# Kernel optimization log

Hardware: AMD Instinct MI355X
Metric: run time of the kernel (lower is better)

The kernel has to match this reference:

```python
import jax, jax.numpy as jnp
import numpy as np

B, T, K = 256, 1024, 128


def setup_inputs() -> dict:
    key = jax.random.key(0)
    k1, k2, k3, k4, k5 = jax.random.split(key, 5)
    EMISSIONS = jax.random.normal(k1, (B, T, K), dtype=jnp.float32)
    TAGS = jax.random.randint(k2, (B, T), 0, K, dtype=jnp.int64)
    MASK = jnp.ones((B, T), dtype=bool)
    START = jax.random.normal(k3, (K,), dtype=jnp.float32) * 0.01
    END = jax.random.normal(k4, (K,), dtype=jnp.float32) * 0.01
    TRANS = jax.random.normal(k5, (K, K), dtype=jnp.float32) * 0.01
    return {"EMISSIONS": EMISSIONS, "TAGS": TAGS, "MASK": MASK,
            "START": START, "END": END, "TRANS": TRANS}


def _forward_logz(emissions, mask, start, end, trans):
    # emissions (B,T,K), mask (B,T) bool -> logZ (B,)
    alpha0 = start[None, :] + emissions[:, 0, :]  # (B,K)

    def step(alpha, inp):
        emit, m = inp  # emit (B,K), m (B,) bool
        # PACK[b,i,j] = alpha[b,i] + trans[i,j]; logsumexp over prev tag i
        new = jax.nn.logsumexp(alpha[:, :, None] + trans[None, :, :], axis=1) + emit
        alpha = jnp.where(m[:, None], new, alpha)
        return alpha, None

    xs = (jnp.swapaxes(emissions[:, 1:, :], 0, 1),  # (T-1,B,K)
          jnp.swapaxes(mask[:, 1:], 0, 1))          # (T-1,B)
    alphaT, _ = jax.lax.scan(step, alpha0, xs)
    return jax.nn.logsumexp(alphaT + end[None, :], axis=1)


def _gold_score(emissions, tags, mask, start, end, trans):
    b = emissions.shape[0]
    ba = jnp.arange(b)
    maskf = mask.astype(emissions.dtype)
    sc0 = (start[tags[:, 0]] + emissions[ba, 0, tags[:, 0]]) * maskf[:, 0]
    pr = jnp.maximum(tags[:, :-1], 0)  # clamp(min=0)
    cr = jnp.maximum(tags[:, 1:], 0)
    m = (mask[:, 1:] & mask[:, :-1]).astype(emissions.dtype)  # (B,T-1)
    trans_sc = trans[pr, cr]  # (B,T-1)
    emit_sc = jnp.take_along_axis(emissions[:, 1:, :], cr[:, :, None], axis=2)[:, :, 0]
    sc = sc0 + jnp.sum((trans_sc + emit_sc) * m, axis=1)
    lenm1 = jnp.sum(mask.astype(jnp.int32), axis=1) - 1
    last = tags[ba, lenm1]
    return sc + end[last]


def reference(EMISSIONS, TAGS, MASK, START, END, TRANS):
    logz = _forward_logz(EMISSIONS, MASK, START, END, TRANS)
    gold = _gold_score(EMISSIONS, TAGS, MASK, START, END, TRANS)
    return jnp.mean(logz - gold)
```

## Files before the change

kernel.cpp:

```cpp
#include <hip/hip_runtime.h>
#include <math.h>

#define Bn 256
#define Tn 1024
#define Kn 128
#define NT 512
#define CH 16
#define CHF (CH * Kn)
#define USTR 36
#define UW (4 * USTR)

__device__ __forceinline__ float quad_reduce_add(float s) {
    int t = __builtin_amdgcn_mov_dpp(__float_as_int(s), 0xB1, 0xF, 0xF, true);
    s += __int_as_float(t);
    t = __builtin_amdgcn_mov_dpp(__float_as_int(s), 0x4E, 0xF, 0xF, true);
    s += __int_as_float(t);
    return s;
}

__global__ __launch_bounds__(NT, 2) void crf_fwd_kernel(
    const float* __restrict__ emis,
    const int*   __restrict__ tags,
    const float* __restrict__ startv,
    const float* __restrict__ endv,
    const float* __restrict__ trans,
    float* __restrict__ per_b)
{
    const int b    = blockIdx.x;
    const int tid  = threadIdx.x;
    const int wave = tid >> 6;
    const int lane = tid & 63;
    const int c    = wave * 16 + (lane >> 2);
    const int h    = lane & 3;

    __shared__ __align__(16) float U[2][UW];
    __shared__ __align__(16) float X[2][CHF];
    __shared__ float red[NT];

    const float* eb = emis + (size_t)b * Tn * Kn;
    const int*   tb = tags + b * Tn;

    const float* tp = trans + (size_t)(h * 32) * Kn + c;
    float4 E0, E1, E2, E3, E4, E5, E6, E7;
#define LDE(g, Eg)                                   \
    Eg.x = __expf(tp[(size_t)(4 * g + 0) * Kn]);     \
    Eg.y = __expf(tp[(size_t)(4 * g + 1) * Kn]);     \
    Eg.z = __expf(tp[(size_t)(4 * g + 2) * Kn]);     \
    Eg.w = __expf(tp[(size_t)(4 * g + 3) * Kn]);
    LDE(0, E0) LDE(1, E1) LDE(2, E2) LDE(3, E3)
    LDE(4, E4) LDE(5, E5) LDE(6, E6) LDE(7, E7)
#undef LDE

    float gl = 0.f;
    for (int t = 1 + tid; t < Tn; t += NT) {
        int pt = tb[t - 1];
        int ct = tb[t];
        gl += trans[pt * Kn + ct] + eb[(size_t)t * Kn + ct];
    }
    if (tid == 0) {
        int t0 = tb[0];
        gl += startv[t0] + eb[t0] + endv[tb[Tn - 1]];
    }
    red[tid] = gl;

    {
        const float4* e4 = (const float4*)(eb + Kn);
        ((float4*)X[0])[tid] = e4[tid];
    }
    if (tid < Kn) {
        U[1][(tid >> 5) * USTR + (tid & 31)] = __expf(startv[tid] + eb[tid]);
    }
    __syncthreads();

#pragma unroll
    for (int s = NT / 2; s > 0; s >>= 1) {
        if (tid < s) red[tid] += red[tid + s];
        __syncthreads();
    }
    const float gold = red[0];

    float  base = 0.f;
    float4 pf0  = make_float4(0, 0, 0, 0);
    const int urd = h * USTR;
    const int uwr = (c >> 5) * USTR + (c & 31);

    for (int r = 1; r < Tn; ++r) {
        const int tc   = r - 1;
        const int slot = tc & (CH - 1);
        const int cbuf = (tc >> 4) & 1;
        const int rb   = r & 1;
        const int wb   = rb ^ 1;

        if (slot == 0 && r + CH < Tn) {
            const float4* s4 = (const float4*)(eb + (size_t)(r + CH) * Kn);
            size_t base_el = (size_t)(r + CH) * Kn;
            pf0 = (base_el + (size_t)tid * 4 + 3 < (size_t)Tn * Kn)
                      ? s4[tid] : make_float4(0, 0, 0, 0);
        }
        if (slot == 8 && (r - 8) + CH < Tn) {
            ((float4*)X[cbuf ^ 1])[tid] = pf0;
        }

        const float4* Up = (const float4*)&U[rb][urd];
        float u0 = U[rb][0];
        float xr = X[cbuf][slot * Kn + c];

        float4 q0 = Up[0], q1 = Up[1], q2 = Up[2], q3 = Up[3];
        float4 q4 = Up[4], q5 = Up[5], q6 = Up[6], q7 = Up[7];
        float s0 = 0.f, s1 = 0.f, s2 = 0.f, s3 = 0.f;
#define DOT4(q, Eg)                  \
        s0 = fmaf(q.x, Eg.x, s0);    \
        s1 = fmaf(q.y, Eg.y, s1);    \
        s2 = fmaf(q.z, Eg.z, s2);    \
        s3 = fmaf(q.w, Eg.w, s3);
        DOT4(q0, E0) DOT4(q1, E1) DOT4(q2, E2) DOT4(q3, E3)
        DOT4(q4, E4) DOT4(q5, E5) DOT4(q6, E6) DOT4(q7, E7)
#undef DOT4
        float s = (s0 + s1) + (s2 + s3);
        s = quad_reduce_add(s);

        float rn = __builtin_amdgcn_rcpf(u0);
        float qn = (s * __expf(xr)) * rn;
        if (h == 0) U[wb][uwr] = qn;
        if (tid == 0) base += __logf(u0);
        __syncthreads();
    }

    float v = 0.f;
    if (tid < Kn) {
        float uT = U[Tn & 1][(tid >> 5) * USTR + (tid & 31)];
        v = uT * __expf(endv[tid]);
    }
    red[tid] = v;
    __syncthreads();
#pragma unroll
    for (int s = NT / 2; s > 0; s >>= 1) {
        if (tid < s) red[tid] += red[tid + s];
        __syncthreads();
    }
    if (tid == 0)
        per_b[b] = base + __logf(red[0]) - gold;
}

__global__ __launch_bounds__(256) void crf_reduce(const float* __restrict__ per_b,
                                                  float* __restrict__ out) {
    __shared__ float red[256];
    int tid = threadIdx.x;
    red[tid] = per_b[tid];
    __syncthreads();
#pragma unroll
    for (int s = 128; s > 0; s >>= 1) {
        if (tid < s) red[tid] += red[tid + s];
        __syncthreads();
    }
    if (tid == 0) out[0] = red[0] * (1.0f / Bn);
}

extern "C" void kernel_launch(void* const* d_in, const int* in_sizes, int n_in,
                              void* d_out, int out_size, void* d_ws, size_t ws_size,
                              hipStream_t stream) {
    const float* emis   = (const float*)d_in[0];
    const int*   tags   = (const int*)d_in[1];
    const float* startv = (const float*)d_in[3];
    const float* endv   = (const float*)d_in[4];
    const float* trans  = (const float*)d_in[5];

    float* per_b = (float*)d_ws;

    crf_fwd_kernel<<<dim3(Bn), dim3(NT), 0, stream>>>(emis, tags, startv, endv,
                                                      trans, per_b);
    crf_reduce<<<dim3(1), dim3(256), 0, stream>>>(per_b, (float*)d_out);
}
```

Baseline: 564.1 us.

## Remap CRF recurrence to 4 outputs per 16-lane group with row reductions

Each 16-lane row now computes four adjacent output tags, with each lane covering 8 previous tags. U loads per lane shrink from eight float4s to two, and transition rows load as float4. The lane sums are combined with a four-step DPP row reduction on four values, and one lane writes a float4 result. The emission exp moves into the prefetch-to-LDS store, so the serial step avoids an exp. The trade is more DPP reduction work per step and fewer lanes doing the final write.

Result: slower. 645.6 us (+14.4%).

```diff
diff --git a/kernel.cpp b/kernel.cpp
--- a/kernel.cpp
+++ b/kernel.cpp
@@ -7,13 +7,19 @@
 #define NT 512
 #define CH 16
 #define CHF (CH * Kn)
-#define USTR 36
-#define UW (4 * USTR)
+#define CSTR 12
+#define UW (16 * CSTR)
+#define UIDX(j) (((j) >> 3) * CSTR + ((j) & 7))
 
-__device__ __forceinline__ float quad_reduce_add(float s) {
-    int t = __builtin_amdgcn_mov_dpp(__float_as_int(s), 0xB1, 0xF, 0xF, true);
+__device__ __forceinline__ float row16_reduce_add(float s) {
+    int t;
+    t = __builtin_amdgcn_mov_dpp(__float_as_int(s), 0xB1, 0xF, 0xF, true);
     s += __int_as_float(t);
     t = __builtin_amdgcn_mov_dpp(__float_as_int(s), 0x4E, 0xF, 0xF, true);
+    s += __int_as_float(t);
+    t = __builtin_amdgcn_mov_dpp(__float_as_int(s), 0x124, 0xF, 0xF, true);
+    s += __int_as_float(t);
+    t = __builtin_amdgcn_mov_dpp(__float_as_int(s), 0x128, 0xF, 0xF, true);
     s += __int_as_float(t);
     return s;
 }
@@ -30,8 +36,9 @@
     const int tid  = threadIdx.x;
     const int wave = tid >> 6;
     const int lane = tid & 63;
-    const int c    = wave * 16 + (lane >> 2);
-    const int h    = lane & 3;
+    const int hh   = lane & 15;
+    const int g    = lane >> 4;
+    const int c0   = wave * 16 + g * 4;
 
     __shared__ __align__(16) float U[2][UW];
     __shared__ __align__(16) float X[2][CHF];
@@ -40,13 +47,14 @@
     const float* eb = emis + (size_t)b * Tn * Kn;
     const int*   tb = tags + b * Tn;
 
-    const float* tp = trans + (size_t)(h * 32) * Kn + c;
+    const float* tp = trans + (size_t)(8 * hh) * Kn + c0;
     float4 E0, E1, E2, E3, E4, E5, E6, E7;
-#define LDE(g, Eg)                                   \
-    Eg.x = __expf(tp[(size_t)(4 * g + 0) * Kn]);     \
-    Eg.y = __expf(tp[(size_t)(4 * g + 1) * Kn]);     \
-    Eg.z = __expf(tp[(size_t)(4 * g + 2) * Kn]);     \
-    Eg.w = __expf(tp[(size_t)(4 * g + 3) * Kn]);
+#define LDE(k, Ek)                                        \
+    {                                                     \
+        float4 rr = *(const float4*)(tp + (size_t)(k)*Kn);\
+        Ek = make_float4(__expf(rr.x), __expf(rr.y),      \
+                         __expf(rr.z), __expf(rr.w));     \
+    }
     LDE(0, E0) LDE(1, E1) LDE(2, E2) LDE(3, E3)
     LDE(4, E4) LDE(5, E5) LDE(6, E6) LDE(7, E7)
 #undef LDE
@@ -65,10 +73,12 @@
 
     {
         const float4* e4 = (const float4*)(eb + Kn);
-        ((float4*)X[0])[tid] = e4[tid];
+        float4 a = e4[tid];
+        ((float4*)X[0])[tid] =
+            make_float4(__expf(a.x), __expf(a.y), __expf(a.z), __expf(a.w));
     }
     if (tid < Kn) {
-        U[1][(tid >> 5) * USTR + (tid & 31)] = __expf(startv[tid] + eb[tid]);
+        U[1][UIDX(tid)] = __expf(startv[tid] + eb[tid]);
     }
     __syncthreads();
 
@@ -81,8 +91,7 @@
 
     float  base = 0.f;
     float4 pf0  = make_float4(0, 0, 0, 0);
-    const int urd = h * USTR;
-    const int uwr = (c >> 5) * USTR + (c & 31);
+    const int uwr = (c0 >> 3) * CSTR + (c0 & 7);
 
     for (int r = 1; r < Tn; ++r) {
         const int tc   = r - 1;
@@ -98,37 +107,46 @@
                       ? s4[tid] : make_float4(0, 0, 0, 0);
         }
         if (slot == 8 && (r - 8) + CH < Tn) {
-            ((float4*)X[cbuf ^ 1])[tid] = pf0;
+            ((float4*)X[cbuf ^ 1])[tid] =
+                make_float4(__expf(pf0.x), __expf(pf0.y), __expf(pf0.z), __expf(pf0.w));
         }
 
-        const float4* Up = (const float4*)&U[rb][urd];
         float u0 = U[rb][0];
-        float xr = X[cbuf][slot * Kn + c];
+        float4 xv4 = make_float4(0, 0, 0, 0);
+        if (hh == 0)
+            xv4 = ((const float4*)&X[cbuf][slot * Kn])[c0 >> 2];
+        const float4* Up = (const float4*)&U[rb][hh * CSTR];
+        float4 q0 = Up[0];
+        float4 q1 = Up[1];
 
-        float4 q0 = Up[0], q1 = Up[1], q2 = Up[2], q3 = Up[3];
-        float4 q4 = Up[4], q5 = Up[5], q6 = Up[6], q7 = Up[7];
-        float s0 = 0.f, s1 = 0.f, s2 = 0.f, s3 = 0.f;
-#define DOT4(q, Eg)                  \
-        s0 = fmaf(q.x, Eg.x, s0);    \
-        s1 = fmaf(q.y, Eg.y, s1);    \
-        s2 = fmaf(q.z, Eg.z, s2);    \
-        s3 = fmaf(q.w, Eg.w, s3);
-        DOT4(q0, E0) DOT4(q1, E1) DOT4(q2, E2) DOT4(q3, E3)
-        DOT4(q4, E4) DOT4(q5, E5) DOT4(q6, E6) DOT4(q7, E7)
-#undef DOT4
-        float s = (s0 + s1) + (s2 + s3);
-        s = quad_reduce_add(s);
+        float4 s = make_float4(0, 0, 0, 0);
+#define DOT(qc, Ek)                      \
+        s.x = fmaf(qc, Ek.x, s.x);       \
+        s.y = fmaf(qc, Ek.y, s.y);       \
+        s.z = fmaf(qc, Ek.z, s.z);       \
+        s.w = fmaf(qc, Ek.w, s.w);
+        DOT(q0.x, E0) DOT(q0.y, E1) DOT(q0.z, E2) DOT(q0.w, E3)
+        DOT(q1.x, E4) DOT(q1.y, E5) DOT(q1.z, E6) DOT(q1.w, E7)
+#undef DOT
+
+        s.x = row16_reduce_add(s.x);
+        s.y = row16_reduce_add(s.y);
+        s.z = row16_reduce_add(s.z);
+        s.w = row16_reduce_add(s.w);
 
         float rn = __builtin_amdgcn_rcpf(u0);
-        float qn = (s * __expf(xr)) * rn;
-        if (h == 0) U[wb][uwr] = qn;
+        if (hh == 0) {
+            float4 qn = make_float4(s.x * xv4.x * rn, s.y * xv4.y * rn,
+                                    s.z * xv4.z * rn, s.w * xv4.w * rn);
+            *(float4*)&U[wb][uwr] = qn;
+        }
         if (tid == 0) base += __logf(u0);
         __syncthreads();
     }
 
     float v = 0.f;
     if (tid < Kn) {
-        float uT = U[Tn & 1][(tid >> 5) * USTR + (tid & 31)];
+        float uT = U[Tn & 1][UIDX(tid)];
         v = uT * __expf(endv[tid]);
     }
     red[tid] = v;
```
